# Optimization experiments

Hardware: AMD Instinct MI355X
Metric: run time of the kernel (lower is better)

The kernel has to match this reference:

```python
import jax, jax.numpy as jnp
from jax import lax
import numpy as np

NODE_COUNT = 4096
BATCH = 128
THRESHOLD = 1.0
DISSIPATION = 0.1
SPARSITY = 0.9
MAX_ITERS = 100


def setup_inputs() -> dict:
    key = jax.random.key(0)
    k_in, k_conn, k_mask, k_w, k_b = jax.random.split(key, 5)
    input_data = jax.random.normal(k_in, (BATCH, NODE_COUNT), dtype=jnp.float32)
    conn = jax.random.normal(k_conn, (NODE_COUNT, NODE_COUNT), dtype=jnp.float32)
    mask = (jax.random.uniform(k_mask, (NODE_COUNT, NODE_COUNT)) > SPARSITY).astype(jnp.float32)
    conn = conn * mask
    conn = conn / (jnp.abs(conn).sum(axis=1, keepdims=True) + 1e-6)
    # input_proj: Linear(node_count, node_count), torch default init scale
    bound = 1.0 / np.sqrt(NODE_COUNT)
    W = jax.random.uniform(k_w, (NODE_COUNT, NODE_COUNT), minval=-bound, maxval=bound, dtype=jnp.float32)
    b = jax.random.uniform(k_b, (NODE_COUNT,), minval=-bound, maxval=bound, dtype=jnp.float32)
    return {"input_data": input_data, "W": W, "b": b, "connections": conn}


def _avalanche(state, connections):
    """Batched avalanche scan with per-sample sticky early-exit (torch break)."""
    B = state.shape[0]
    done0 = jnp.zeros((B,), dtype=bool)
    total0 = jnp.zeros((B,), dtype=state.dtype)

    def step(carry, _):
        state, done, total = carry
        active = (state > THRESHOLD).astype(state.dtype)          # [B, N]
        n_active = active.sum(axis=1)                              # [B]
        new_done = done | (n_active == 0)                          # break condition
        total = total + jnp.where(new_done, 0.0, n_active)
        # propagated = connections @ active  (per sample)
        prop = jnp.einsum('ij,bj->bi', connections, active)        # [B, N]
        new_state = (state * (1.0 - DISSIPATION) + prop * (1.0 - active)) * (1.0 - active)
        state = jnp.where(new_done[:, None], state, new_state)
        return (state, new_done, total), None

    (state, done, total), _ = lax.scan(step, (state, done0, total0), None, length=MAX_ITERS)
    return state, total


def reference(input_data, W, b, connections):
    projected = input_data @ W.T + b                               # [B, N]
    output, sizes = _avalanche(projected, connections)
    max_size = sizes.max()
    return output, max_size
```

## Files before the change

### kernel.cpp

```cpp
#include <hip/hip_runtime.h>

#define N_NODES 4096
#define BATCH 128
#define SPLITK 16
#define GBN 128
#define GBK 32
#define KCHUNK (N_NODES / SPLITK)
#define NSTEP (KCHUNK / GBK)
#define GEMM_BLOCKS ((N_NODES / GBN) * SPLITK)
#define TRANS_BLOCKS 1024

typedef _Float16 f16x4 __attribute__((ext_vector_type(4)));
typedef _Float16 f16x8 __attribute__((ext_vector_type(8)));
typedef float f32x4 __attribute__((ext_vector_type(4)));
typedef unsigned int u32x4 __attribute__((ext_vector_type(4)));

__device__ __forceinline__ void dma16(const void* g, void* l) {
#if defined(__has_builtin) && __has_builtin(__builtin_amdgcn_global_load_lds)
  __builtin_amdgcn_global_load_lds((const __attribute__((address_space(1))) void*)g,
                                   (__attribute__((address_space(3))) void*)l, 16, 0, 0);
#else
  *(u32x4*)l = *(const u32x4*)g;
#endif
}

#if defined(__has_builtin)
#if __has_builtin(__builtin_amdgcn_cvt_f32_fp8) && __has_builtin(__builtin_amdgcn_cvt_pk_fp8_f32)
#define CONN_FP8 1
#endif
#endif
#ifndef CONN_FP8
#define CONN_FP8 0
#endif

#if CONN_FP8
#define CONN_ELEM_BYTES 1
#define CONN_SCALE (1.0f / 256.0f)
#else
#define CONN_ELEM_BYTES 2
#define CONN_SCALE 1.0f
#endif

__device__ __forceinline__ void conn_store4(void* out, size_t off, float4 v) {
#if CONN_FP8
  unsigned int p = __builtin_amdgcn_cvt_pk_fp8_f32(v.x * 256.0f, v.y * 256.0f, 0, false);
  p = (unsigned int)__builtin_amdgcn_cvt_pk_fp8_f32(v.z * 256.0f, v.w * 256.0f, (int)p, true);
  *(unsigned int*)((unsigned char*)out + off) = p;
#else
  const unsigned int ux = __float_as_uint(v.x), uy = __float_as_uint(v.y);
  const unsigned int uz = __float_as_uint(v.z), uw = __float_as_uint(v.w);
  ushort4 u;
  u.x = (unsigned short)((ux + 0x7FFFu + ((ux >> 16) & 1u)) >> 16);
  u.y = (unsigned short)((uy + 0x7FFFu + ((uy >> 16) & 1u)) >> 16);
  u.z = (unsigned short)((uz + 0x7FFFu + ((uz >> 16) & 1u)) >> 16);
  u.w = (unsigned short)((uw + 0x7FFFu + ((uw >> 16) & 1u)) >> 16);
  *(ushort4*)((unsigned short*)out + off) = u;
#endif
}

__device__ __forceinline__ float4 conn_load4(const void* cT, int j, int t) {
#if CONN_FP8
  const unsigned int c = *(const unsigned int*)((const unsigned char*)cT + ((size_t)j << 12) + t * 4);
  return make_float4(__builtin_amdgcn_cvt_f32_fp8(c, 0), __builtin_amdgcn_cvt_f32_fp8(c, 1),
                     __builtin_amdgcn_cvt_f32_fp8(c, 2), __builtin_amdgcn_cvt_f32_fp8(c, 3));
#else
  const ushort4 c = *(const ushort4*)((const unsigned short*)cT + ((size_t)j << 12) + t * 4);
  return make_float4(__uint_as_float((unsigned int)c.x << 16),
                     __uint_as_float((unsigned int)c.y << 16),
                     __uint_as_float((unsigned int)c.z << 16),
                     __uint_as_float((unsigned int)c.w << 16));
#endif
}

__global__ __launch_bounds__(256) void asplit_kernel(const float* __restrict__ in,
                                                     _Float16* __restrict__ As,
                                                     unsigned int* __restrict__ maxslot) {
  if (blockIdx.x == 0 && threadIdx.x == 0) *maxslot = 0u;
  const size_t idx = ((size_t)blockIdx.x * 256 + threadIdx.x) * 4;
  const int m = (int)(idx >> 12);
  const int k = (int)(idx & (N_NODES - 1));
  const float4 v = *(const float4*)(in + idx);
  f16x4 hi, lo;
  const float x0 = v.x * 256.f, x1 = v.y * 256.f, x2 = v.z * 256.f, x3 = v.w * 256.f;
  hi[0] = (_Float16)x0; lo[0] = (_Float16)(x0 - (float)hi[0]);
  hi[1] = (_Float16)x1; lo[1] = (_Float16)(x1 - (float)hi[1]);
  hi[2] = (_Float16)x2; lo[2] = (_Float16)(x2 - (float)hi[2]);
  hi[3] = (_Float16)x3; lo[3] = (_Float16)(x3 - (float)hi[3]);
  const size_t base = (size_t)m * 8192 + (size_t)(k >> 5) * 64 + (k & 31);
  *(f16x4*)(As + base) = hi;
  *(f16x4*)(As + base + 32) = lo;
}

struct GemmSmem {
  alignas(16) _Float16 A[2][128 * 64];
  alignas(16) float B[2][128 * 32];
};
struct TransSmem { float tile[4][64][65]; };
union PrepSmem { GemmSmem g; TransSmem t; };

__global__ __launch_bounds__(256, 2) void fused_prep_kernel(
    const _Float16* __restrict__ As, const float* __restrict__ W,
    const float* __restrict__ conn, float* __restrict__ P, void* __restrict__ connT) {
  __shared__ PrepSmem sm;
  const int tid = threadIdx.x;
  const int bid = blockIdx.x;
  const int wave = tid >> 6, lane = tid & 63;

  if (bid < GEMM_BLOCKS) {
    const int wm = wave >> 1, wn = wave & 1;
    const int g = lane >> 4, lrow = lane & 15;
    const int n0 = (bid & 31) * GBN;
    const int kb = (bid >> 5) * KCHUNK;
    const int crow = lane >> 3;
    const int q = lane & 7;

    auto issue = [&](int buf, int t) {
      const size_t abyte = (size_t)((kb >> 5) + t) * 128;
      const size_t bbyte = (size_t)(kb + t * GBK) * 4;
#pragma unroll
      for (int i = 0; i < 4; ++i) {
        const int c = wave * 4 + i;
        const int row = c * 8 + crow;
        dma16((const char*)As + (size_t)row * 16384 + abyte + ((q ^ crow) << 4),
              (char*)sm.g.A[buf] + c * 1024 + lane * 16);
      }
#pragma unroll
      for (int i = 0; i < 4; ++i) {
        const int c = wave * 4 + i;
        const int row = c * 8 + crow;
        dma16((const char*)W + (size_t)(n0 + row) * 16384 + bbyte + ((q ^ crow) << 4),
              (char*)sm.g.B[buf] + c * 1024 + lane * 16);
      }
    };

    f32x4 acc[4][4] = {};
    issue(0, 0);
    issue(1, 1);

#pragma unroll
    for (int t = 0; t < NSTEP; ++t) {
      const int cur = t & 1;
      if (t + 1 < NSTEP) asm volatile("s_waitcnt vmcnt(8)" ::: "memory");
      else               asm volatile("s_waitcnt vmcnt(0)" ::: "memory");
      __builtin_amdgcn_sched_barrier(0);
      __builtin_amdgcn_s_barrier();
      __builtin_amdgcn_sched_barrier(0);

      f16x8 ah[4], al[4];
#pragma unroll
      for (int fm = 0; fm < 4; ++fm) {
        const int mr = wm * 64 + fm * 16 + lrow;
        const char* ab = (const char*)sm.g.A[cur] + mr * 128;
        const int s = (mr & 7) << 4;
        ah[fm] = *(const f16x8*)(ab + ((g << 4) ^ s));
        al[fm] = *(const f16x8*)(ab + (((4 + g) << 4) ^ s));
      }
      f16x8 bh[4], bl[4];
#pragma unroll
      for (int fn = 0; fn < 4; ++fn) {
        const int nr = wn * 64 + fn * 16 + lrow;
        const char* bb = (const char*)sm.g.B[cur] + nr * 128;
        const int s = (nr & 7) << 4;
        const f32x4 b0 = *(const f32x4*)(bb + (((2 * g) << 4) ^ s));
        const f32x4 b1 = *(const f32x4*)(bb + (((2 * g + 1) << 4) ^ s));
#pragma unroll
        for (int j = 0; j < 4; ++j) {
          const float x = b0[j] * 64.f;
          const _Float16 h = (_Float16)x;
          bh[fn][j] = h; bl[fn][j] = (_Float16)(x - (float)h);
          const float y = b1[j] * 64.f;
          const _Float16 h2 = (_Float16)y;
          bh[fn][4 + j] = h2; bl[fn][4 + j] = (_Float16)(y - (float)h2);
        }
      }
#pragma unroll
      for (int fm = 0; fm < 4; ++fm)
#pragma unroll
        for (int fn = 0; fn < 4; ++fn) {
          acc[fm][fn] = __builtin_amdgcn_mfma_f32_16x16x32_f16(ah[fm], bh[fn], acc[fm][fn], 0, 0, 0);
          acc[fm][fn] = __builtin_amdgcn_mfma_f32_16x16x32_f16(ah[fm], bl[fn], acc[fm][fn], 0, 0, 0);
          acc[fm][fn] = __builtin_amdgcn_mfma_f32_16x16x32_f16(al[fm], bh[fn], acc[fm][fn], 0, 0, 0);
        }

      __builtin_amdgcn_sched_barrier(0);
      __builtin_amdgcn_s_barrier();
      __builtin_amdgcn_sched_barrier(0);
      if (t + 2 < NSTEP) issue(cur, t + 2);
    }

    constexpr float INV = 1.0f / 16384.0f;
    float* Pb = P + (size_t)(bid >> 5) * BATCH * N_NODES;
#pragma unroll
    for (int fm = 0; fm < 4; ++fm)
#pragma unroll
      for (int fn = 0; fn < 4; ++fn) {
        const int n = n0 + wn * 64 + fn * 16 + lrow;
#pragma unroll
        for (int reg = 0; reg < 4; ++reg) {
          const int m = wm * 64 + fm * 16 + g * 4 + reg;
          Pb[(size_t)m * N_NODES + n] = acc[fm][fn][reg] * INV;
        }
      }
  } else {
    const int tile_id = (bid - GEMM_BLOCKS) * 4 + wave;
    const int bx = tile_id & 63, by = tile_id >> 6;
    float (*T)[65] = sm.t.tile[wave];
    const int lr = lane >> 4;
    const int lc = lane & 15;
#pragma unroll
    for (int i = 0; i < 16; ++i) {
      const int r = lr + 4 * i;
      const float4 v = *(const float4*)(conn + (size_t)(by * 64 + r) * N_NODES + bx * 64 + lc * 4);
      T[r][lc * 4 + 0] = v.x; T[r][lc * 4 + 1] = v.y;
      T[r][lc * 4 + 2] = v.z; T[r][lc * 4 + 3] = v.w;
    }
#pragma unroll
    for (int i = 0; i < 16; ++i) {
      const int orow = lr + 4 * i;
      float4 v;
      v.x = T[lc * 4 + 0][orow];
      v.y = T[lc * 4 + 1][orow];
      v.z = T[lc * 4 + 2][orow];
      v.w = T[lc * 4 + 3][orow];
      conn_store4(connT, (size_t)(bx * 64 + orow) * N_NODES + by * 64 + lc * 4, v);
    }
  }
}

__global__ __launch_bounds__(256) void proj_gemm_valu(const float* __restrict__ A,
                                                      const float* __restrict__ W,
                                                      float* __restrict__ P,
                                                      unsigned int* __restrict__ maxslot) {
  if (blockIdx.x == 0 && threadIdx.x == 0) *maxslot = 0u;
  __shared__ float Asb[16][132];
  __shared__ float Bsb[16][68];
  const int tid = threadIdx.x;
  const int n0 = blockIdx.x * 64;
  const int tx = tid & 15, ty = tid >> 4;
  const int arow = tid >> 1, acol = (tid & 1) * 8;
  const int brow = tid >> 2, bcol = (tid & 3) * 4;
  float acc[2][4][4] = {};
  const float* Aptr = A + (size_t)arow * N_NODES + acol;
  const float* Wptr = W + (size_t)(n0 + brow) * N_NODES + bcol;
  for (int k0 = 0; k0 < N_NODES; k0 += 16) {
    const float4 a0 = *(const float4*)(Aptr + k0);
    const float4 a1 = *(const float4*)(Aptr + k0 + 4);
    const float4 bv = *(const float4*)(Wptr + k0);
    __syncthreads();
    Asb[acol + 0][arow] = a0.x; Asb[acol + 1][arow] = a0.y;
    Asb[acol + 2][arow] = a0.z; Asb[acol + 3][arow] = a0.w;
    Asb[acol + 4][arow] = a1.x; Asb[acol + 5][arow] = a1.y;
    Asb[acol + 6][arow] = a1.z; Asb[acol + 7][arow] = a1.w;
    Bsb[bcol + 0][brow] = bv.x; Bsb[bcol + 1][brow] = bv.y;
    Bsb[bcol + 2][brow] = bv.z; Bsb[bcol + 3][brow] = bv.w;
    __syncthreads();
#pragma unroll
    for (int kk = 0; kk < 16; ++kk) {
      const float4 av0 = *(const float4*)&Asb[kk][ty * 4];
      const float4 av1 = *(const float4*)&Asb[kk][64 + ty * 4];
      const float4 bv4 = *(const float4*)&Bsb[kk][tx * 4];
      const float am[8] = {av0.x, av0.y, av0.z, av0.w, av1.x, av1.y, av1.z, av1.w};
      const float bn[4] = {bv4.x, bv4.y, bv4.z, bv4.w};
#pragma unroll
      for (int i2 = 0; i2 < 2; ++i2)
#pragma unroll
        for (int i = 0; i < 4; ++i)
#pragma unroll
          for (int j = 0; j < 4; ++j)
            acc[i2][i][j] += am[i2 * 4 + i] * bn[j];
    }
  }
#pragma unroll
  for (int i2 = 0; i2 < 2; ++i2)
#pragma unroll
    for (int i = 0; i < 4; ++i) {
      const int m = i2 * 64 + ty * 4 + i;
      *(float4*)(P + (size_t)m * N_NODES + n0 + tx * 4) =
          make_float4(acc[i2][i][0], acc[i2][i][1], acc[i2][i][2], acc[i2][i][3]);
    }
}

__global__ __launch_bounds__(256) void bias_inplace_kernel(float* __restrict__ P,
                                                           const float* __restrict__ bias) {
  const size_t base = ((size_t)blockIdx.x * 256 + threadIdx.x) * 4;
  const int n = (int)(base & (N_NODES - 1));
  float4 s = *(const float4*)(P + base);
  const float4 bv = *(const float4*)(bias + n);
  s.x += bv.x; s.y += bv.y; s.z += bv.z; s.w += bv.w;
  *(float4*)(P + base) = s;
}

template <int MODE, int NSPLIT>
__global__ __launch_bounds__(1024) void avalanche_kernel(const float* __restrict__ Pin,
                                                         const float* __restrict__ bias,
                                                         const void* __restrict__ connv,
                                                         float* __restrict__ out,
                                                         unsigned int* __restrict__ maxslot) {
  const int b = blockIdx.x;
  const int t = threadIdx.x;
  __shared__ unsigned long long mask[64];
  __shared__ int wincl[64];
  __shared__ int list[N_NODES];

  float4 s;
  if (MODE == 1) {
    const float4 bv = *(const float4*)(bias + t * 4);
    s = bv;
#pragma unroll
    for (int sp = 0; sp < NSPLIT; ++sp) {
      const float4 v = *(const float4*)(Pin + (size_t)sp * BATCH * N_NODES +
                                        (size_t)b * N_NODES + t * 4);
      s.x += v.x; s.y += v.y; s.z += v.z; s.w += v.w;
    }
  } else {
    s = *(const float4*)(Pin + (size_t)b * N_NODES + t * 4);
  }

  float total = 0.0f;

  for (int it = 0; it < 100; ++it) {
    const float v0 = s.x, v1 = s.y, v2 = s.z, v3 = s.w;
    unsigned int bits = 0;
    if (v0 > 1.0f) bits |= 1u;
    if (v1 > 1.0f) bits |= 2u;
    if (v2 > 1.0f) bits |= 4u;
    if (v3 > 1.0f) bits |= 8u;

    __syncthreads();
    if (t < 64) mask[t] = 0ULL;
    __syncthreads();
    if (bits) atomicOr(&mask[t >> 4], (unsigned long long)bits << ((t & 15) * 4));
    __syncthreads();

    if (t < 64) {
      int incl = __popcll(mask[t]);
#pragma unroll
      for (int d = 1; d < 64; d <<= 1) {
        const int y = __shfl_up(incl, d);
        if (t >= d) incl += y;
      }
      wincl[t] = incl;
    }
    __syncthreads();
    const int n = wincl[63];
    if (n == 0) break;
    total += (float)n;

    if (t < 64) {
      unsigned long long m = mask[t];
      int o = wincl[t] - __popcll(m);
      while (m) {
        list[o++] = (t << 6) + __builtin_ctzll(m);
        m &= m - 1;
      }
    }
    __syncthreads();

    float4 a0 = make_float4(0.f, 0.f, 0.f, 0.f), a1 = a0, a2 = a0, a3 = a0;
    if (MODE == 1) {
      int idx = 0;
      for (; idx + 8 <= n; idx += 8) {
        const float4 c0 = conn_load4(connv, list[idx + 0], t);
        const float4 c1 = conn_load4(connv, list[idx + 1], t);
        const float4 c2 = conn_load4(connv, list[idx + 2], t);
        const float4 c3 = conn_load4(connv, list[idx + 3], t);
        const float4 c4 = conn_load4(connv, list[idx + 4], t);
        const float4 c5 = conn_load4(connv, list[idx + 5], t);
        const float4 c6 = conn_load4(connv, list[idx + 6], t);
        const float4 c7 = conn_load4(connv, list[idx + 7], t);
        a0.x += c0.x; a0.y += c0.y; a0.z += c0.z; a0.w += c0.w;
        a1.x += c1.x; a1.y += c1.y; a1.z += c1.z; a1.w += c1.w;
        a2.x += c2.x; a2.y += c2.y; a2.z += c2.z; a2.w += c2.w;
        a3.x += c3.x; a3.y += c3.y; a3.z += c3.z; a3.w += c3.w;
        a0.x += c4.x; a0.y += c4.y; a0.z += c4.z; a0.w += c4.w;
        a1.x += c5.x; a1.y += c5.y; a1.z += c5.z; a1.w += c5.w;
        a2.x += c6.x; a2.y += c6.y; a2.z += c6.z; a2.w += c6.w;
        a3.x += c7.x; a3.y += c7.y; a3.z += c7.z; a3.w += c7.w;
      }
      for (; idx < n; ++idx) {
        const float4 c = conn_load4(connv, list[idx], t);
        a0.x += c.x; a0.y += c.y; a0.z += c.z; a0.w += c.w;
      }
    } else {
      const float* conn = (const float*)connv;
      for (int idx = 0; idx < n; ++idx) {
        const int j = list[idx];
        a0.x += conn[(size_t)(t * 4 + 0) * N_NODES + j];
        a0.y += conn[(size_t)(t * 4 + 1) * N_NODES + j];
        a0.z += conn[(size_t)(t * 4 + 2) * N_NODES + j];
        a0.w += conn[(size_t)(t * 4 + 3) * N_NODES + j];
      }
    }
    const float sc = (MODE == 1) ? CONN_SCALE : 1.0f;
    const float4 acc = make_float4(((a0.x + a1.x) + (a2.x + a3.x)) * sc,
                                   ((a0.y + a1.y) + (a2.y + a3.y)) * sc,
                                   ((a0.z + a1.z) + (a2.z + a3.z)) * sc,
                                   ((a0.w + a1.w) + (a2.w + a3.w)) * sc);

    s.x = (v0 > 1.0f) ? 0.0f : 0.9f * v0 + acc.x;
    s.y = (v1 > 1.0f) ? 0.0f : 0.9f * v1 + acc.y;
    s.z = (v2 > 1.0f) ? 0.0f : 0.9f * v2 + acc.z;
    s.w = (v3 > 1.0f) ? 0.0f : 0.9f * v3 + acc.w;
  }

  *(float4*)(out + (size_t)b * N_NODES + t * 4) = s;
  if (t == 0) atomicMax(maxslot, __float_as_uint(total));
}

extern "C" void kernel_launch(void* const* d_in, const int* in_sizes, int n_in,
                              void* d_out, int out_size, void* d_ws, size_t ws_size,
                              hipStream_t stream) {
  const float* input = (const float*)d_in[0];
  const float* W     = (const float*)d_in[1];
  const float* bias  = (const float*)d_in[2];
  const float* conn  = (const float*)d_in[3];
  float* out = (float*)d_out;

  const size_t aplane_bytes = (size_t)BATCH * N_NODES * 4;
  const size_t connT_bytes  = (size_t)N_NODES * N_NODES * CONN_ELEM_BYTES;
  const size_t part_bytes   = (size_t)SPLITK * BATCH * N_NODES * sizeof(float);
  unsigned int* maxslot = (unsigned int*)(out + (size_t)BATCH * N_NODES);

  if (ws_size >= aplane_bytes + connT_bytes + part_bytes) {
    _Float16* As = (_Float16*)d_ws;
    void* connT  = (char*)d_ws + aplane_bytes;
    float* part  = (float*)((char*)d_ws + aplane_bytes + connT_bytes);
    asplit_kernel<<<BATCH * N_NODES / 1024, 256, 0, stream>>>(input, As, maxslot);
    fused_prep_kernel<<<GEMM_BLOCKS + TRANS_BLOCKS, 256, 0, stream>>>(As, W, conn, part, connT);
    avalanche_kernel<1, SPLITK><<<BATCH, 1024, 0, stream>>>(part, bias, connT, out, maxslot);
  } else {
    proj_gemm_valu<<<dim3(N_NODES / 64, 1), 256, 0, stream>>>(input, W, out, maxslot);
    bias_inplace_kernel<<<BATCH * N_NODES / 1024, 256, 0, stream>>>(out, bias);
    avalanche_kernel<0, 1><<<BATCH, 1024, 0, stream>>>(out, nullptr, conn, out, maxslot);
  }
}
```

Baseline: 69.50 us.

## Split fused prep into separate transpose and GEMM kernels with swizzled block order

Splits the fused GEMM and transpose kernel into two launches. The transpose now uses 128x128 tiles per block with float4 LDS writes, and the GEMM uses a block-index remap that groups neighbouring N tiles and K chunks, which should improve L2 locality. The GEMM also raises wave priority around the MFMA section with s_setprio. In exchange it loses the overlap between transpose and GEMM blocks inside one launch and adds an extra kernel launch.

```diff
diff --git a/kernel.cpp b/kernel.cpp
--- a/kernel.cpp
+++ b/kernel.cpp
@@ -8,7 +8,7 @@
 #define KCHUNK (N_NODES / SPLITK)
 #define NSTEP (KCHUNK / GBK)
 #define GEMM_BLOCKS ((N_NODES / GBN) * SPLITK)
-#define TRANS_BLOCKS 1024
+#define TRANS_BLOCKS (32 * 32)
 
 typedef _Float16 f16x4 __attribute__((ext_vector_type(4)));
 typedef _Float16 f16x8 __attribute__((ext_vector_type(8)));
@@ -91,140 +91,151 @@
   *(f16x4*)(As + base + 32) = lo;
 }
 
+__global__ __launch_bounds__(256, 2) void transpose_kernel(const float* __restrict__ conn,
+                                                           void* __restrict__ connT) {
+  __shared__ float T[128][129];
+  const int tid = threadIdx.x;
+  const int d = blockIdx.x;
+  const int by = (d & 7) | ((d >> 8) << 3);
+  const int bx = (d >> 3) & 31;
+
+  const int rr = tid >> 4;
+  const int c0 = (tid & 15) * 4;
+#pragma unroll
+  for (int pass = 0; pass < 8; ++pass) {
+    const int r = pass * 16 + rr;
+    const float* src = conn + (size_t)(by * 128 + r) * N_NODES + bx * 128;
+    const float4 a = *(const float4*)(src + c0);
+    const float4 b = *(const float4*)(src + c0 + 64);
+    *(float4*)&T[r][c0] = a;
+    *(float4*)&T[r][c0 + 64] = b;
+  }
+  __syncthreads();
+
+  const int jr = tid >> 5;
+  const int lc = tid & 31;
+#pragma unroll
+  for (int pass = 0; pass < 16; ++pass) {
+    const int jj = pass * 8 + jr;
+    float4 v;
+    v.x = T[lc * 4 + 0][jj];
+    v.y = T[lc * 4 + 1][jj];
+    v.z = T[lc * 4 + 2][jj];
+    v.w = T[lc * 4 + 3][jj];
+    conn_store4(connT, (size_t)(bx * 128 + jj) * N_NODES + by * 128 + lc * 4, v);
+  }
+}
+
 struct GemmSmem {
   alignas(16) _Float16 A[2][128 * 64];
   alignas(16) float B[2][128 * 32];
 };
-struct TransSmem { float tile[4][64][65]; };
-union PrepSmem { GemmSmem g; TransSmem t; };
-
-__global__ __launch_bounds__(256, 2) void fused_prep_kernel(
-    const _Float16* __restrict__ As, const float* __restrict__ W,
-    const float* __restrict__ conn, float* __restrict__ P, void* __restrict__ connT) {
-  __shared__ PrepSmem sm;
+
+__global__ __launch_bounds__(256, 2) void gemm_kernel(const _Float16* __restrict__ As,
+                                                      const float* __restrict__ W,
+                                                      float* __restrict__ P) {
+  __shared__ GemmSmem sm;
   const int tid = threadIdx.x;
-  const int bid = blockIdx.x;
+  const int d = blockIdx.x;
+  const int ntile = (d & 7) | ((d >> 7) << 3);
+  const int kidx = (d >> 3) & 15;
   const int wave = tid >> 6, lane = tid & 63;
-
-  if (bid < GEMM_BLOCKS) {
-    const int wm = wave >> 1, wn = wave & 1;
-    const int g = lane >> 4, lrow = lane & 15;
-    const int n0 = (bid & 31) * GBN;
-    const int kb = (bid >> 5) * KCHUNK;
-    const int crow = lane >> 3;
-    const int q = lane & 7;
-
-    auto issue = [&](int buf, int t) {
-      const size_t abyte = (size_t)((kb >> 5) + t) * 128;
-      const size_t bbyte = (size_t)(kb + t * GBK) * 4;
-#pragma unroll
-      for (int i = 0; i < 4; ++i) {
-        const int c = wave * 4 + i;
-        const int row = c * 8 + crow;
-        dma16((const char*)As + (size_t)row * 16384 + abyte + ((q ^ crow) << 4),
-              (char*)sm.g.A[buf] + c * 1024 + lane * 16);
-      }
-#pragma unroll
-      for (int i = 0; i < 4; ++i) {
-        const int c = wave * 4 + i;
-        const int row = c * 8 + crow;
-        dma16((const char*)W + (size_t)(n0 + row) * 16384 + bbyte + ((q ^ crow) << 4),
-              (char*)sm.g.B[buf] + c * 1024 + lane * 16);
-      }
-    };
-
-    f32x4 acc[4][4] = {};
-    issue(0, 0);
-    issue(1, 1);
-
-#pragma unroll
-    for (int t = 0; t < NSTEP; ++t) {
-      const int cur = t & 1;
-      if (t + 1 < NSTEP) asm volatile("s_waitcnt vmcnt(8)" ::: "memory");
-      else               asm volatile("s_waitcnt vmcnt(0)" ::: "memory");
-      __builtin_amdgcn_sched_barrier(0);
-      __builtin_amdgcn_s_barrier();
-      __builtin_amdgcn_sched_barrier(0);
-
-      f16x8 ah[4], al[4];
-#pragma unroll
-      for (int fm = 0; fm < 4; ++fm) {
-        const int mr = wm * 64 + fm * 16 + lrow;
-        const char* ab = (const char*)sm.g.A[cur] + mr * 128;
-        const int s = (mr & 7) << 4;
-        ah[fm] = *(const f16x8*)(ab + ((g << 4) ^ s));
-        al[fm] = *(const f16x8*)(ab + (((4 + g) << 4) ^ s));
-      }
-      f16x8 bh[4], bl[4];
+  const int wm = wave >> 1, wn = wave & 1;
+  const int g = lane >> 4, lrow = lane & 15;
+  const int n0 = ntile * GBN;
+  const int kb = kidx * KCHUNK;
+  const int crow = lane >> 3;
+  const int q = lane & 7;
+
+  auto issue = [&](int buf, int t) {
+    const size_t abyte = (size_t)((kb >> 5) + t) * 128;
+    const size_t bbyte = (size_t)(kb + t * GBK) * 4;
+#pragma unroll
+    for (int i = 0; i < 4; ++i) {
+      const int c = wave * 4 + i;
+      const int row = c * 8 + crow;
+      dma16((const char*)As + (size_t)row * 16384 + abyte + ((q ^ crow) << 4),
+            (char*)sm.A[buf] + c * 1024 + lane * 16);
+    }
+#pragma unroll
+    for (int i = 0; i < 4; ++i) {
+      const int c = wave * 4 + i;
+      const int row = c * 8 + crow;
+      dma16((const char*)W + (size_t)(n0 + row) * 16384 + bbyte + ((q ^ crow) << 4),
+            (char*)sm.B[buf] + c * 1024 + lane * 16);
+    }
+  };
+
+  f32x4 acc[4][4] = {};
+  issue(0, 0);
+  issue(1, 1);
+
+#pragma unroll
+  for (int t = 0; t < NSTEP; ++t) {
+    const int cur = t & 1;
+    if (t + 1 < NSTEP) asm volatile("s_waitcnt vmcnt(8)" ::: "memory");
+    else               asm volatile("s_waitcnt vmcnt(0)" ::: "memory");
+    __builtin_amdgcn_sched_barrier(0);
+    __builtin_amdgcn_s_barrier();
+    __builtin_amdgcn_sched_barrier(0);
+
+    f16x8 ah[4], al[4];
+#pragma unroll
+    for (int fm = 0; fm < 4; ++fm) {
+      const int mr = wm * 64 + fm * 16 + lrow;
+      const char* ab = (const char*)sm.A[cur] + mr * 128;
+      const int s = (mr & 7) << 4;
+      ah[fm] = *(const f16x8*)(ab + ((g << 4) ^ s));
+      al[fm] = *(const f16x8*)(ab + (((4 + g) << 4) ^ s));
+    }
+    f16x8 bh[4], bl[4];
+#pragma unroll
+    for (int fn = 0; fn < 4; ++fn) {
+      const int nr = wn * 64 + fn * 16 + lrow;
+      const char* bb = (const char*)sm.B[cur] + nr * 128;
+      const int s = (nr & 7) << 4;
+      const f32x4 b0 = *(const f32x4*)(bb + (((2 * g) << 4) ^ s));
+      const f32x4 b1 = *(const f32x4*)(bb + (((2 * g + 1) << 4) ^ s));
+#pragma unroll
+      for (int j = 0; j < 4; ++j) {
+        const float x = b0[j] * 64.f;
+        const _Float16 h = (_Float16)x;
+        bh[fn][j] = h; bl[fn][j] = (_Float16)(x - (float)h);
+        const float y = b1[j] * 64.f;
+        const _Float16 h2 = (_Float16)y;
+        bh[fn][4 + j] = h2; bl[fn][4 + j] = (_Float16)(y - (float)h2);
+      }
+    }
+    __builtin_amdgcn_s_setprio(1);
+#pragma unroll
+    for (int fm = 0; fm < 4; ++fm)
 #pragma unroll
       for (int fn = 0; fn < 4; ++fn) {
-        const int nr = wn * 64 + fn * 16 + lrow;
-        const char* bb = (const char*)sm.g.B[cur] + nr * 128;
-        const int s = (nr & 7) << 4;
-        const f32x4 b0 = *(const f32x4*)(bb + (((2 * g) << 4) ^ s));
-        const f32x4 b1 = *(const f32x4*)(bb + (((2 * g + 1) << 4) ^ s));
-#pragma unroll
-        for (int j = 0; j < 4; ++j) {
-          const float x = b0[j] * 64.f;
-          const _Float16 h = (_Float16)x;
-          bh[fn][j] = h; bl[fn][j] = (_Float16)(x - (float)h);
-          const float y = b1[j] * 64.f;
-          const _Float16 h2 = (_Float16)y;
-          bh[fn][4 + j] = h2; bl[fn][4 + j] = (_Float16)(y - (float)h2);
-        }
-      }
-#pragma unroll
-      for (int fm = 0; fm < 4; ++fm)
-#pragma unroll
-        for (int fn = 0; fn < 4; ++fn) {
-          acc[fm][fn] = __builtin_amdgcn_mfma_f32_16x16x32_f16(ah[fm], bh[fn], acc[fm][fn], 0, 0, 0);
-          acc[fm][fn] = __builtin_amdgcn_mfma_f32_16x16x32_f16(ah[fm], bl[fn], acc[fm][fn], 0, 0, 0);
-          acc[fm][fn] = __builtin_amdgcn_mfma_f32_16x16x32_f16(al[fm], bh[fn], acc[fm][fn], 0, 0, 0);
-        }
-
-      __builtin_amdgcn_sched_barrier(0);
-      __builtin_amdgcn_s_barrier();
-      __builtin_amdgcn_sched_barrier(0);
-      if (t + 2 < NSTEP) issue(cur, t + 2);
-    }
-
-    constexpr float INV = 1.0f / 16384.0f;
-    float* Pb = P + (size_t)(bid >> 5) * BATCH * N_NODES;
-#pragma unroll
-    for (int fm = 0; fm < 4; ++fm)
-#pragma unroll
-      for (int fn = 0; fn < 4; ++fn) {
-        const int n = n0 + wn * 64 + fn * 16 + lrow;
-#pragma unroll
-        for (int reg = 0; reg < 4; ++reg) {
-          const int m = wm * 64 + fm * 16 + g * 4 + reg;
-          Pb[(size_t)m * N_NODES + n] = acc[fm][fn][reg] * INV;
-        }
-      }
-  } else {
-    const int tile_id = (bid - GEMM_BLOCKS) * 4 + wave;
-    const int bx = tile_id & 63, by = tile_id >> 6;
-    float (*T)[65] = sm.t.tile[wave];
-    const int lr = lane >> 4;
-    const int lc = lane & 15;
-#pragma unroll
-    for (int i = 0; i < 16; ++i) {
-      const int r = lr + 4 * i;
-      const float4 v = *(const float4*)(conn + (size_t)(by * 64 + r) * N_NODES + bx * 64 + lc * 4);
-      T[r][lc * 4 + 0] = v.x; T[r][lc * 4 + 1] = v.y;
-      T[r][lc * 4 + 2] = v.z; T[r][lc * 4 + 3] = v.w;
-    }
-#pragma unroll
-    for (int i = 0; i < 16; ++i) {
-      const int orow = lr + 4 * i;
-      float4 v;
-      v.x = T[lc * 4 + 0][orow];
-      v.y = T[lc * 4 + 1][orow];
-      v.z = T[lc * 4 + 2][orow];
-      v.w = T[lc * 4 + 3][orow];
-      conn_store4(connT, (size_t)(bx * 64 + orow) * N_NODES + by * 64 + lc * 4, v);
-    }
-  }
+        acc[fm][fn] = __builtin_amdgcn_mfma_f32_16x16x32_f16(ah[fm], bh[fn], acc[fm][fn], 0, 0, 0);
+        acc[fm][fn] = __builtin_amdgcn_mfma_f32_16x16x32_f16(ah[fm], bl[fn], acc[fm][fn], 0, 0, 0);
+        acc[fm][fn] = __builtin_amdgcn_mfma_f32_16x16x32_f16(al[fm], bh[fn], acc[fm][fn], 0, 0, 0);
+      }
+    __builtin_amdgcn_s_setprio(0);
+
+    __builtin_amdgcn_sched_barrier(0);
+    __builtin_amdgcn_s_barrier();
+    __builtin_amdgcn_sched_barrier(0);
+    if (t + 2 < NSTEP) issue(cur, t + 2);
+  }
+
+  constexpr float INV = 1.0f / 16384.0f;
+  float* Pb = P + (size_t)kidx * BATCH * N_NODES;
+#pragma unroll
+  for (int fm = 0; fm < 4; ++fm)
+#pragma unroll
+    for (int fn = 0; fn < 4; ++fn) {
+      const int n = n0 + wn * 64 + fn * 16 + lrow;
+#pragma unroll
+      for (int reg = 0; reg < 4; ++reg) {
+        const int m = wm * 64 + fm * 16 + g * 4 + reg;
+        Pb[(size_t)m * N_NODES + n] = acc[fm][fn][reg] * INV;
+      }
+    }
 }
 
 __global__ __launch_bounds__(256) void proj_gemm_valu(const float* __restrict__ A,
@@ -426,7 +437,8 @@
     void* connT  = (char*)d_ws + aplane_bytes;
     float* part  = (float*)((char*)d_ws + aplane_bytes + connT_bytes);
     asplit_kernel<<<BATCH * N_NODES / 1024, 256, 0, stream>>>(input, As, maxslot);
-    fused_prep_kernel<<<GEMM_BLOCKS + TRANS_BLOCKS, 256, 0, stream>>>(As, W, conn, part, connT);
+    transpose_kernel<<<TRANS_BLOCKS, 256, 0, stream>>>(conn, connT);
+    gemm_kernel<<<GEMM_BLOCKS, 256, 0, stream>>>(As, W, part);
     avalanche_kernel<1, SPLITK><<<BATCH, 1024, 0, stream>>>(part, bias, connT, out, maxslot);
   } else {
     proj_gemm_valu<<<dim3(N_NODES / 64, 1), 256, 0, stream>>>(input, W, out, maxslot);
```

After: 71.34 us. +2.7%, slower.
